# Kernel tuning notes

Measured on AMD Instinct MI355X. Metric: run time of the kernel, lower is better.

Reference implementation:

```python
import jax, jax.numpy as jnp
import numpy as np

R, NU, NM, E = 5, 100000, 100000, 1000000
IN, MSG, OUT, BAS = 64, 80, 64, 4
MPR = MSG // R  # per-rating message units (stack agg)


def setup_inputs() -> dict:
    key = jax.random.key(0)
    ks = jax.random.split(key, 12)
    return {
        "ufeat": jax.random.normal(ks[0], (NU, IN), jnp.float32),
        "ifeat": jax.random.normal(ks[1], (NM, IN), jnp.float32),
        "cj_user": jax.random.uniform(ks[2], (NU, 1), jnp.float32) + 0.1,
        "ci_user": jax.random.uniform(ks[3], (NU, 1), jnp.float32) + 0.1,
        "cj_movie": jax.random.uniform(ks[4], (NM, 1), jnp.float32) + 0.1,
        "ci_movie": jax.random.uniform(ks[5], (NM, 1), jnp.float32) + 0.1,
        "edge_user": jax.random.randint(ks[6], (R, E), 0, NU, jnp.int32),
        "edge_movie": jax.random.randint(ks[7], (R, E), 0, NM, jnp.int32),
        "att": jax.random.normal(ks[8], (R, BAS), jnp.float32),
        "basis": jax.random.normal(ks[9], (BAS, IN, MPR), jnp.float32),
        "fc_w": jax.random.normal(ks[10], (OUT, MSG), jnp.float32) / np.sqrt(MSG),
        "fc_b": jnp.zeros((OUT,), jnp.float32),
    }


def _agg(feat, src, dst, cj, ci, n_dst):
    # gather src features scaled by cj, scatter-sum to dst, scale by ci
    m = feat[src] * cj[src]                                 # [E, MPR]
    out = jax.ops.segment_sum(m, dst, num_segments=n_dst)   # [n_dst, MPR]
    return out * ci


def reference(ufeat, ifeat, cj_user, ci_user, cj_movie, ci_movie,
              edge_user, edge_movie, att, basis, fc_w, fc_b):
    # per-rating weights from basis decomposition
    W = jnp.einsum('rb,bio->rio', att, basis)       # [R, IN, MPR]
    fu = jnp.einsum('ni,rio->rno', ufeat, W)        # [R, NU, MPR]
    fi = jnp.einsum('ni,rio->rno', ifeat, W)        # [R, NM, MPR]
    agg = jax.vmap(_agg, in_axes=(0, 0, 0, None, None, None))
    # forward edges: user -> movie; reverse edges: movie -> user
    m_out = agg(fu, edge_user, edge_movie, cj_user, ci_movie, NM)  # [R, NM, MPR]
    u_out = agg(fi, edge_movie, edge_user, cj_movie, ci_user, NU)  # [R, NU, MPR]
    # 'stack' cross-type aggregation, flattened over ratings
    u = jnp.transpose(u_out, (1, 0, 2)).reshape(NU, MSG)
    m = jnp.transpose(m_out, (1, 0, 2)).reshape(NM, MSG)
    u = jax.nn.relu(u) @ fc_w.T + fc_b   # shared ufc == ifc
    m = jax.nn.relu(m) @ fc_w.T + fc_b
    return u, m
```

## Files before the change

### kernel.cpp

```cpp
#include <hip/hip_runtime.h>
#include <cstdint>
#include <cstddef>

constexpr int kR   = 5;
constexpr int kNU  = 100000;
constexpr int kNM  = 100000;
constexpr int kE   = 1000000;
constexpr int kIN  = 64;
constexpr int kMSG = 80;
constexpr int kOUT = 64;
constexpr int kBAS = 4;
constexpr int kMPR = 16;

constexpr int kN        = 100000;
constexpr unsigned kEdges   = (unsigned)kR * (unsigned)kE;

constexpr int kBD        = 50;
constexpr int kNB        = kN / kBD;

constexpr int kNC        = 2;
constexpr unsigned kPlanesPerChunk = 250000;
constexpr int kBinsPerDir = kNB * kNC;
constexpr unsigned kCap2 = 1536;
constexpr int kChunkE    = 16384;
constexpr int kDirBlocks = (int)((kEdges + kChunkE - 1) / kChunkE);
constexpr int kMsgBlocks = (kN + 255) / 256;

constexpr float kScale    = 64.0f;
constexpr float kInvScale = 1.0f / 64.0f;

constexpr int kStride = 17;
constexpr int kAccWords = kBD * kR * kStride;

__global__ __launch_bounds__(256) void gcmc_init(
    uint32_t* __restrict__ cursor, const float* __restrict__ fc_w,
    float* __restrict__ Wq)
{
    const int t = blockIdx.x * 256 + threadIdx.x;
    if (t < 2 * kBinsPerDir) cursor[t] = (uint32_t)t * kCap2;
    if (t < 20 * kOUT * 4) {
        const int q  = t & 3;
        const int o  = (t >> 2) & 63;
        const int j4 = t >> 8;
        Wq[t] = fc_w[o * kMSG + j4 * 4 + q];
    }
}

__device__ __forceinline__ uint32_t pack2i16(float x, float y) {
    const int ix = (int)rintf(fminf(fmaxf(x, -32760.f), 32760.f));
    const int iy = (int)rintf(fminf(fmaxf(y, -32760.f), 32760.f));
    return (uint32_t)(ix & 0xFFFF) | ((uint32_t)(iy & 0xFFFF) << 16);
}

__global__ __launch_bounds__(256) void gcmc_msg(
    const float* __restrict__ ufeat, const float* __restrict__ ifeat,
    const float* __restrict__ cj_user, const float* __restrict__ cj_movie,
    const float* __restrict__ att,  const float* __restrict__ basis,
    short* __restrict__ ms)
{
    __shared__ float Wl[kR * kIN * kMPR];
    const int tid  = threadIdx.x;
    const int side = blockIdx.x >= kMsgBlocks;
    const int blk  = blockIdx.x - side * kMsgBlocks;
    const float* feat = side ? ifeat : ufeat;
    const float* cj   = side ? cj_movie : cj_user;
    uint2* mout = reinterpret_cast<uint2*>(ms + (side ? (size_t)kR * kN * kMPR : 0));

    for (int idx = tid; idx < kR * kIN * kMPR; idx += 256) {
        const int r   = idx >> 10;
        const int rem = idx & 1023;
        const int i   = rem >> 4;
        const int k   = rem & 15;
        float s = 0.f;
#pragma unroll
        for (int b = 0; b < kBAS; ++b)
            s += att[r * kBAS + b] * basis[(b * kIN + i) * kMPR + k];
        Wl[idx] = s;
    }
    __syncthreads();

    const int node = blk * 256 + tid;
    if (node >= kN) return;

    float f[kIN];
    const float4* fp = reinterpret_cast<const float4*>(feat + (size_t)node * kIN);
#pragma unroll
    for (int i = 0; i < kIN / 4; ++i) {
        float4 v = fp[i];
        f[4 * i + 0] = v.x; f[4 * i + 1] = v.y;
        f[4 * i + 2] = v.z; f[4 * i + 3] = v.w;
    }
    const float c = cj[node] * kScale;
    const float4* W4 = reinterpret_cast<const float4*>(Wl);

    for (int r = 0; r < kR; ++r) {
#pragma unroll
        for (int kg = 0; kg < kMPR / 4; ++kg) {
            float4 a = make_float4(0.f, 0.f, 0.f, 0.f);
#pragma unroll
            for (int i = 0; i < kIN; ++i) {
                float4 w = W4[(r * kIN + i) * (kMPR / 4) + kg];
                a.x += f[i] * w.x; a.y += f[i] * w.y;
                a.z += f[i] * w.z; a.w += f[i] * w.w;
            }
            const uint32_t plane = (uint32_t)(r * kN + node);
            mout[plane * 4u + kg] =
                make_uint2(pack2i16(a.x * c, a.y * c), pack2i16(a.z * c, a.w * c));
        }
    }
}

__global__ __launch_bounds__(1024) void gcmc_partition(
    const int* __restrict__ dst0, const int* __restrict__ src0,
    const int* __restrict__ dst1, const int* __restrict__ src1,
    uint32_t* __restrict__ cursor, uint32_t* __restrict__ bucket_recs)
{
    __shared__ uint32_t hist[kBinsPerDir];
    __shared__ uint32_t excl[kBinsPerDir];
    __shared__ uint32_t scanT[1024];
    __shared__ uint32_t stage[kChunkE];
    __shared__ uint16_t sbkt[kChunkE];
    const int tid = threadIdx.x;
    const int dir = blockIdx.x >= kDirBlocks;
    const int blk = blockIdx.x - dir * kDirBlocks;
    const int* dsts = dir ? dst1 : dst0;
    const int* srcs = dir ? src1 : src0;

    for (int i = tid; i < kBinsPerDir; i += 1024) hist[i] = 0;
    __syncthreads();

    const unsigned base = (unsigned)blk * kChunkE;
    uint32_t rec[16], bk[16], rk[16];
#pragma unroll
    for (int j = 0; j < 16; ++j) {
        const unsigned idx = base + j * 1024u + tid;
        if (idx < kEdges) {
            const unsigned d = (unsigned)dsts[idx];
            const unsigned s = (unsigned)srcs[idx];
            const unsigned r = idx / (unsigned)kE;
            const unsigned b = d / (unsigned)kBD;
            const unsigned dl = d - b * (unsigned)kBD;
            const unsigned plane = r * (unsigned)kN + s;
            const unsigned ch = plane / kPlanesPerChunk;
            const unsigned binl = b * (unsigned)kNC + ch;
            rec[j] = plane | (((dl * (unsigned)kR + r) * 17u) << 19);
            bk[j]  = binl;
            rk[j]  = atomicAdd(&hist[binl], 1u);
        } else bk[j] = 0xFFFFFFFFu;
    }
    __syncthreads();

    uint32_t loc[4]; uint32_t s2 = 0;
#pragma unroll
    for (int q = 0; q < 4; ++q) {
        const int b = tid * 4 + q;
        loc[q] = (b < kBinsPerDir) ? hist[b] : 0u;
        s2 += loc[q];
    }
    scanT[tid] = s2; __syncthreads();
    for (int off = 1; off < 1024; off <<= 1) {
        const uint32_t v = (tid >= off) ? scanT[tid - off] : 0u;
        __syncthreads();
        scanT[tid] += v;
        __syncthreads();
    }
    const uint32_t total = scanT[1023];
    uint32_t run = scanT[tid] - s2;
#pragma unroll
    for (int q = 0; q < 4; ++q) {
        const int b = tid * 4 + q;
        if (b < kBinsPerDir) {
            excl[b] = run;
            hist[b] = loc[q] ? atomicAdd(&cursor[dir * kBinsPerDir + b], loc[q]) : 0u;
        }
        run += loc[q];
    }
    __syncthreads();

#pragma unroll
    for (int j = 0; j < 16; ++j) {
        if (bk[j] != 0xFFFFFFFFu) {
            const uint32_t p = excl[bk[j]] + rk[j];
            stage[p] = rec[j];
            sbkt[p]  = (uint16_t)bk[j];
        }
    }
    __syncthreads();

    for (unsigned p = tid; p < total; p += 1024) {
        const uint32_t b = sbkt[p];
        bucket_recs[hist[b] + (p - excl[b])] = stage[p];
    }
}

__global__ __launch_bounds__(256, 8) void gcmc_accum_fc(
    const short* __restrict__ ms,
    const uint32_t* __restrict__ bucket_recs,
    const uint32_t* __restrict__ cursor,
    const float* __restrict__ ci_user, const float* __restrict__ ci_movie,
    const float* __restrict__ Wq, const float* __restrict__ fc_b,
    float* __restrict__ out_u, float* __restrict__ out_m)
{
    __shared__ int accI[kAccWords];
    const int tid = threadIdx.x;
    const int db  = blockIdx.x;
    const int dir = db >= kNB;
    const int bl  = db - dir * kNB;

    for (int i = tid; i < kAccWords; i += 256) accI[i] = 0;
    __syncthreads();

    const uint4* pb = reinterpret_cast<const uint4*>(
        ms + (dir ? (size_t)kR * kN * kMPR : 0));

#define RRR(IDX) { const uint32_t rc = rp[(IDX)];                           \
                   const uint4* lp = pb + (size_t)(rc & 0x7FFFFu) * 2u;      \
                   const uint4 va = lp[0];                                   \
                   const uint4 vb = lp[1];                                   \
                   const int w = (int)(rc >> 19);                            \
                   atomicAdd(&accI[w+ 0], (int)(short)va.x);                 \
                   atomicAdd(&accI[w+ 1], ((int)va.x) >> 16);                \
                   atomicAdd(&accI[w+ 2], (int)(short)va.y);                 \
                   atomicAdd(&accI[w+ 3], ((int)va.y) >> 16);                \
                   atomicAdd(&accI[w+ 4], (int)(short)va.z);                 \
                   atomicAdd(&accI[w+ 5], ((int)va.z) >> 16);                \
                   atomicAdd(&accI[w+ 6], (int)(short)va.w);                 \
                   atomicAdd(&accI[w+ 7], ((int)va.w) >> 16);                \
                   atomicAdd(&accI[w+ 8], (int)(short)vb.x);                 \
                   atomicAdd(&accI[w+ 9], ((int)vb.x) >> 16);                \
                   atomicAdd(&accI[w+10], (int)(short)vb.y);                 \
                   atomicAdd(&accI[w+11], ((int)vb.y) >> 16);                \
                   atomicAdd(&accI[w+12], (int)(short)vb.z);                 \
                   atomicAdd(&accI[w+13], ((int)vb.z) >> 16);                \
                   atomicAdd(&accI[w+14], (int)(short)vb.w);                 \
                   atomicAdd(&accI[w+15], ((int)vb.w) >> 16); }

    for (int ch = 0; ch < kNC; ++ch) {
        const int bin = (dir * kBinsPerDir) + bl * kNC + ch;
        const uint32_t b0 = (uint32_t)bin * kCap2;
        const uint32_t n  = cursor[bin] - b0;
        const uint32_t* rp = bucket_recs + b0;
        uint32_t i = (uint32_t)tid;
        for (; i + 768u < n; i += 1024u) { RRR(i) RRR(i + 256u) RRR(i + 512u) RRR(i + 768u) }
        for (; i < n; i += 256u) { RRR(i) }
    }
#undef RRR
    __syncthreads();

    const int o = tid & 63;
    const int w4 = tid >> 6;
    const float* cip = dir ? ci_user : ci_movie;
    float* outp      = dir ? out_u  : out_m;
    const int dstBase = bl * kBD;
    const float bo = fc_b[o];
    const float4* Wq4 = reinterpret_cast<const float4*>(Wq);

    for (int dl = w4; dl < kBD; dl += 4) {
        const float cs = cip[dstBase + dl] * kInvScale;
        float a = bo;
#pragma unroll 4
        for (int j4 = 0; j4 < kMSG / 4; ++j4) {
            const int base2 = (dl * kR + (j4 >> 2)) * kStride + ((j4 & 3) << 2);
            const float x0 = fmaxf((float)accI[base2 + 0] * cs, 0.f);
            const float x1 = fmaxf((float)accI[base2 + 1] * cs, 0.f);
            const float x2 = fmaxf((float)accI[base2 + 2] * cs, 0.f);
            const float x3 = fmaxf((float)accI[base2 + 3] * cs, 0.f);
            const float4 wv = Wq4[j4 * 64 + o];
            a += x0 * wv.x + x1 * wv.y + x2 * wv.z + x3 * wv.w;
        }
        outp[(size_t)(dstBase + dl) * kOUT + o] = a;
    }
}

extern "C" void kernel_launch(void* const* d_in, const int* in_sizes, int n_in,
                              void* d_out, int out_size, void* d_ws, size_t ws_size,
                              hipStream_t stream) {
    const float* ufeat    = (const float*)d_in[0];
    const float* ifeat    = (const float*)d_in[1];
    const float* cj_user  = (const float*)d_in[2];
    const float* ci_user  = (const float*)d_in[3];
    const float* cj_movie = (const float*)d_in[4];
    const float* ci_movie = (const float*)d_in[5];
    const int*   edge_user  = (const int*)d_in[6];
    const int*   edge_movie = (const int*)d_in[7];
    const float* att   = (const float*)d_in[8];
    const float* basis = (const float*)d_in[9];
    const float* fc_w  = (const float*)d_in[10];
    const float* fc_b  = (const float*)d_in[11];

    float* out_u = (float*)d_out;
    float* out_m = out_u + (size_t)kNU * kOUT;

    short* ms = (short*)d_ws;
    uint32_t* bucket_recs = (uint32_t*)(ms + (size_t)2 * kR * kN * kMPR);
    uint32_t* cursorC     = bucket_recs + (size_t)(2 * kBinsPerDir) * kCap2;
    float*    Wq          = (float*)(cursorC + 2 * kBinsPerDir);

    gcmc_init<<<40, 256, 0, stream>>>(cursorC, fc_w, Wq);

    gcmc_msg<<<2 * kMsgBlocks, 256, 0, stream>>>(
        ufeat, ifeat, cj_user, cj_movie, att, basis, ms);

    gcmc_partition<<<2 * kDirBlocks, 1024, 0, stream>>>(
        edge_movie, edge_user, edge_user, edge_movie, cursorC, bucket_recs);

    gcmc_accum_fc<<<2 * kNB, 256, 0, stream>>>(
        ms, bucket_recs, cursorC, ci_user, ci_movie,
        Wq, fc_b, out_u, out_m);
}
```

Before: 350.3 us.

## Collapse per-block source-plane sub-bins into a single bucket per destination block

Edge partitioning now uses one bucket per destination block, with a larger fixed capacity, instead of two sub-bins split by source plane range. This shrinks the histogram and scan work, the cursor count and the per-block bin loop in the accumulate kernel. The cost is losing the source-range grouping that may have helped cache locality of message gathers. The scale and ReLU are also applied once over the shared accumulator in a separate pass before the FC, rather than being redone inside the FC loop, at the price of an extra shared-memory pass and barrier.

```diff
diff --git a/kernel.cpp b/kernel.cpp
--- a/kernel.cpp
+++ b/kernel.cpp
@@ -17,11 +17,7 @@
 
 constexpr int kBD        = 50;
 constexpr int kNB        = kN / kBD;
-
-constexpr int kNC        = 2;
-constexpr unsigned kPlanesPerChunk = 250000;
-constexpr int kBinsPerDir = kNB * kNC;
-constexpr unsigned kCap2 = 1536;
+constexpr unsigned kCap  = 2944;
 constexpr int kChunkE    = 16384;
 constexpr int kDirBlocks = (int)((kEdges + kChunkE - 1) / kChunkE);
 constexpr int kMsgBlocks = (kN + 255) / 256;
@@ -37,7 +33,7 @@
     float* __restrict__ Wq)
 {
     const int t = blockIdx.x * 256 + threadIdx.x;
-    if (t < 2 * kBinsPerDir) cursor[t] = (uint32_t)t * kCap2;
+    if (t < 2 * kNB) cursor[t] = (uint32_t)t * kCap;
     if (t < 20 * kOUT * 4) {
         const int q  = t & 3;
         const int o  = (t >> 2) & 63;
@@ -115,8 +111,8 @@
     const int* __restrict__ dst1, const int* __restrict__ src1,
     uint32_t* __restrict__ cursor, uint32_t* __restrict__ bucket_recs)
 {
-    __shared__ uint32_t hist[kBinsPerDir];
-    __shared__ uint32_t excl[kBinsPerDir];
+    __shared__ uint32_t hist[kNB];
+    __shared__ uint32_t excl[kNB];
     __shared__ uint32_t scanT[1024];
     __shared__ uint32_t stage[kChunkE];
     __shared__ uint16_t sbkt[kChunkE];
@@ -126,7 +122,7 @@
     const int* dsts = dir ? dst1 : dst0;
     const int* srcs = dir ? src1 : src0;
 
-    for (int i = tid; i < kBinsPerDir; i += 1024) hist[i] = 0;
+    for (int i = tid; i < kNB; i += 1024) hist[i] = 0;
     __syncthreads();
 
     const unsigned base = (unsigned)blk * kChunkE;
@@ -140,23 +136,17 @@
             const unsigned r = idx / (unsigned)kE;
             const unsigned b = d / (unsigned)kBD;
             const unsigned dl = d - b * (unsigned)kBD;
-            const unsigned plane = r * (unsigned)kN + s;
-            const unsigned ch = plane / kPlanesPerChunk;
-            const unsigned binl = b * (unsigned)kNC + ch;
-            rec[j] = plane | (((dl * (unsigned)kR + r) * 17u) << 19);
-            bk[j]  = binl;
-            rk[j]  = atomicAdd(&hist[binl], 1u);
+            rec[j] = (r * (unsigned)kN + s) | (((dl * (unsigned)kR + r) * 17u) << 19);
+            bk[j]  = b;
+            rk[j]  = atomicAdd(&hist[b], 1u);
         } else bk[j] = 0xFFFFFFFFu;
     }
     __syncthreads();
 
-    uint32_t loc[4]; uint32_t s2 = 0;
-#pragma unroll
-    for (int q = 0; q < 4; ++q) {
-        const int b = tid * 4 + q;
-        loc[q] = (b < kBinsPerDir) ? hist[b] : 0u;
-        s2 += loc[q];
-    }
+    const int b0 = tid * 2, b1i = tid * 2 + 1;
+    const uint32_t loc0 = (b0 < kNB) ? hist[b0] : 0u;
+    const uint32_t loc1 = (b1i < kNB) ? hist[b1i] : 0u;
+    const uint32_t s2 = loc0 + loc1;
     scanT[tid] = s2; __syncthreads();
     for (int off = 1; off < 1024; off <<= 1) {
         const uint32_t v = (tid >= off) ? scanT[tid - off] : 0u;
@@ -165,15 +155,14 @@
         __syncthreads();
     }
     const uint32_t total = scanT[1023];
-    uint32_t run = scanT[tid] - s2;
-#pragma unroll
-    for (int q = 0; q < 4; ++q) {
-        const int b = tid * 4 + q;
-        if (b < kBinsPerDir) {
-            excl[b] = run;
-            hist[b] = loc[q] ? atomicAdd(&cursor[dir * kBinsPerDir + b], loc[q]) : 0u;
-        }
-        run += loc[q];
+    const uint32_t run = scanT[tid] - s2;
+    if (b0 < kNB) {
+        excl[b0] = run;
+        hist[b0] = loc0 ? atomicAdd(&cursor[dir * kNB + b0], loc0) : 0u;
+    }
+    if (b1i < kNB) {
+        excl[b1i] = run + loc0;
+        hist[b1i] = loc1 ? atomicAdd(&cursor[dir * kNB + b1i], loc1) : 0u;
     }
     __syncthreads();
 
@@ -235,10 +224,9 @@
                    atomicAdd(&accI[w+14], (int)(short)vb.w);                 \
                    atomicAdd(&accI[w+15], ((int)vb.w) >> 16); }
 
-    for (int ch = 0; ch < kNC; ++ch) {
-        const int bin = (dir * kBinsPerDir) + bl * kNC + ch;
-        const uint32_t b0 = (uint32_t)bin * kCap2;
-        const uint32_t n  = cursor[bin] - b0;
+    {
+        const uint32_t b0 = (uint32_t)db * kCap;
+        const uint32_t n  = cursor[db] - b0;
         const uint32_t* rp = bucket_recs + b0;
         uint32_t i = (uint32_t)tid;
         for (; i + 768u < n; i += 1024u) { RRR(i) RRR(i + 256u) RRR(i + 512u) RRR(i + 768u) }
@@ -247,24 +235,35 @@
 #undef RRR
     __syncthreads();
 
+    const float* cip = dir ? ci_user : ci_movie;
+    const int dstBase = bl * kBD;
+    float* accF = reinterpret_cast<float*>(accI);
+    for (int e = tid; e < kAccWords; e += 256) {
+        const int q = e / kStride;
+        const int w = e - q * kStride;
+        if (w < 16) {
+            const int dl = q / kR;
+            const float cs = cip[dstBase + dl] * kInvScale;
+            accF[e] = fmaxf((float)accI[e] * cs, 0.f);
+        }
+    }
+    __syncthreads();
+
     const int o = tid & 63;
     const int w4 = tid >> 6;
-    const float* cip = dir ? ci_user : ci_movie;
-    float* outp      = dir ? out_u  : out_m;
-    const int dstBase = bl * kBD;
+    float* outp = dir ? out_u : out_m;
     const float bo = fc_b[o];
     const float4* Wq4 = reinterpret_cast<const float4*>(Wq);
 
     for (int dl = w4; dl < kBD; dl += 4) {
-        const float cs = cip[dstBase + dl] * kInvScale;
         float a = bo;
 #pragma unroll 4
         for (int j4 = 0; j4 < kMSG / 4; ++j4) {
             const int base2 = (dl * kR + (j4 >> 2)) * kStride + ((j4 & 3) << 2);
-            const float x0 = fmaxf((float)accI[base2 + 0] * cs, 0.f);
-            const float x1 = fmaxf((float)accI[base2 + 1] * cs, 0.f);
-            const float x2 = fmaxf((float)accI[base2 + 2] * cs, 0.f);
-            const float x3 = fmaxf((float)accI[base2 + 3] * cs, 0.f);
+            const float x0 = accF[base2 + 0];
+            const float x1 = accF[base2 + 1];
+            const float x2 = accF[base2 + 2];
+            const float x3 = accF[base2 + 3];
             const float4 wv = Wq4[j4 * 64 + o];
             a += x0 * wv.x + x1 * wv.y + x2 * wv.z + x3 * wv.w;
         }
@@ -293,10 +292,10 @@
 
     short* ms = (short*)d_ws;
     uint32_t* bucket_recs = (uint32_t*)(ms + (size_t)2 * kR * kN * kMPR);
-    uint32_t* cursorC     = bucket_recs + (size_t)(2 * kBinsPerDir) * kCap2;
-    float*    Wq          = (float*)(cursorC + 2 * kBinsPerDir);
-
-    gcmc_init<<<40, 256, 0, stream>>>(cursorC, fc_w, Wq);
+    uint32_t* cursorC     = bucket_recs + (size_t)(2 * kNB) * kCap;
+    float*    Wq          = (float*)(cursorC + 2 * kNB);
+
+    gcmc_init<<<20, 256, 0, stream>>>(cursorC, fc_w, Wq);
 
     gcmc_msg<<<2 * kMsgBlocks, 256, 0, stream>>>(
         ufeat, ifeat, cj_user, cj_movie, att, basis, ms);
```

Measured after the change: 362.1 us. 1.03x slower.
